# Performance work log

Hardware: AMD Instinct MI355X
Metric: run time of the kernel (lower is better)

Reference implementation:

```python
import jax, jax.numpy as jnp
import numpy as np

B = 64      # batch
T = 32      # frames per clip
H = 256     # hidden_dim
NMAX = 64   # max boxes per batch element


def _n_per_frame():
    rng = np.random.default_rng(0)
    return rng.integers(32, NMAX + 1, size=B)  # each n <= NMAX


def setup_inputs() -> dict:
    n = _n_per_frame()
    N = int(n.sum())  # total boxes across batch (~3072)
    key = jax.random.key(0)
    k1, k2, k3 = jax.random.split(key, 3)
    bbox = jax.random.uniform(k1, (N * T, 4), dtype=jnp.float32)
    W1 = jax.random.normal(k2, (4, 128), dtype=jnp.float32) * 0.5
    b1 = jnp.zeros((128,), jnp.float32)
    W2 = jax.random.normal(k3, (128, H), dtype=jnp.float32) * 0.0884  # ~1/sqrt(128)
    b2 = jnp.zeros((H,), jnp.float32)
    return {
        "bbox": bbox,
        "W1": W1, "b1": b1, "W2": W2, "b2": b2,
        "n_per_frame": jnp.asarray(n, jnp.int32),
        "n_max": NMAX,
    }


def reference(bbox, W1, b1, W2, b2, n_per_frame, n_max):
    N = bbox.shape[0] // T  # static total box count
    # tiny MLP: 4 -> 128 -> H
    pos = (jax.nn.relu(bbox @ W1 + b1) @ W2 + b2).reshape(N, T, H)
    # ragged scatter into padded (B*n_max, T, H) tensor
    frame_id = jnp.repeat(jnp.arange(B), n_per_frame, total_repeat_length=N)  # [N]
    starts = jnp.cumsum(n_per_frame) - n_per_frame                            # exclusive cumsum [B]
    local = jnp.arange(N) - starts[frame_id]                                  # slot within frame
    tgt = frame_id * n_max + local                                            # [N] unique targets
    pos_pad = jnp.zeros((B * n_max, T, H), pos.dtype).at[tgt].set(pos)
    # (B, n_max, T, H) -> (B, T, n_max, H) -> (B*T, n_max, H) -> (n_max, B*T, H)
    out = (pos_pad.reshape(B, n_max, T, H)
           .transpose(0, 2, 1, 3)
           .reshape(B * T, n_max, H)
           .transpose(1, 0, 2))
    return out
```

## Files before the change

### kernel.cpp

```cpp
#include <hip/hip_runtime.h>

#define B_ 64
#define T_ 32
#define H_ 256
#define HID_ 128
#define NMAX_ 64
#define TILES 2048
#define GRID 512
#define BLOCK 256

typedef __attribute__((ext_vector_type(8))) short short8;
typedef __attribute__((ext_vector_type(4))) float f32x4;

__device__ __forceinline__ short f2bf(float f) {
    unsigned u = __builtin_bit_cast(unsigned, f);
    u = (u + 0x7fffu + ((u >> 16) & 1u)) >> 16;
    return (short)u;
}

__global__ __launch_bounds__(BLOCK, 2)
void pe_fused(const float* __restrict__ bbox,
              const float* __restrict__ W1,
              const float* __restrict__ b1,
              const float* __restrict__ W2,
              const float* __restrict__ b2,
              const int*   __restrict__ npf,
              float* __restrict__ out,
              int NT)
{
    __shared__ float W1s[512];
    __shared__ float b1s[128];
    __shared__ short Hs[64 * 136];

    const int tid  = threadIdx.x;
    const int wave = tid >> 6;
    const int lane = tid & 63;
    const int q    = lane >> 4;
    const int m16  = lane & 15;

    if (tid < 256) { W1s[tid] = W1[tid]; W1s[tid + 256] = W1[tid + 256]; }
    if (tid < 128) b1s[tid] = b1[tid];

    short8 Bf[4][4];
    float  b2v[4];
#pragma unroll
    for (int ct = 0; ct < 4; ++ct) {
        const int n = wave * 64 + ct * 16 + m16;
        b2v[ct] = b2[n];
#pragma unroll
        for (int kc = 0; kc < 4; ++kc) {
            const int k0 = kc * 32 + q * 8;
            short8 f;
#pragma unroll
            for (int jj = 0; jj < 8; ++jj)
                f[jj] = f2bf(W2[(k0 + jj) * H_ + n]);
            Bf[ct][kc] = f;
        }
    }
    __syncthreads();

    const int r4 = tid >> 2;
    const int c4 = tid & 3;

    for (int tt = blockIdx.x; tt < TILES; tt += GRID) {
        const int b  = tt >> 5;
        const int j  = tt & 31;
        const int nb = npf[b];
        const int l0 = 2 * j;

        const int ob0 = (l0 * (B_ * T_) + b * T_) * H_;
        const int ob1 = ob0 + (B_ * T_) * H_;

        if (l0 >= nb) {
            const int s = r4 >> 5, t = r4 & 31;
            float* dst = out + (s ? ob1 : ob0) + t * H_ + c4 * 64;
            const float4 z = make_float4(0.f, 0.f, 0.f, 0.f);
#pragma unroll
            for (int w = 0; w < 16; ++w)
                *(float4*)(dst + w * 4) = z;
            continue;
        }

        int sb = 0;
        for (int x = 0; x < b; ++x) sb += npf[x];

        {
            const int gr = (sb + l0) * T_ + r4;
            float4 bb = make_float4(0.f, 0.f, 0.f, 0.f);
            if (gr < NT) bb = *(const float4*)(bbox + gr * 4);
#pragma unroll
            for (int w = 0; w < 4; ++w) {
                short8 hv;
#pragma unroll
                for (int jj = 0; jj < 8; ++jj) {
                    const int h = c4 * 32 + w * 8 + jj;
                    float v = b1s[h];
                    v = fmaf(bb.x, W1s[h],       v);
                    v = fmaf(bb.y, W1s[128 + h], v);
                    v = fmaf(bb.z, W1s[256 + h], v);
                    v = fmaf(bb.w, W1s[384 + h], v);
                    v = fmaxf(v, 0.f);
                    hv[jj] = f2bf(v);
                }
                *(short8*)&Hs[r4 * 136 + c4 * 32 + w * 8] = hv;
            }
        }
        __syncthreads();

        f32x4 acc[4][4];
#pragma unroll
        for (int rt = 0; rt < 4; ++rt)
#pragma unroll
            for (int ct = 0; ct < 4; ++ct)
                acc[rt][ct] = (f32x4){0.f, 0.f, 0.f, 0.f};

#pragma unroll
        for (int kc = 0; kc < 4; ++kc) {
            short8 a[4];
#pragma unroll
            for (int rt = 0; rt < 4; ++rt)
                a[rt] = *(const short8*)&Hs[(rt * 16 + m16) * 136 + kc * 32 + q * 8];
#pragma unroll
            for (int rt = 0; rt < 4; ++rt)
#pragma unroll
                for (int ct = 0; ct < 4; ++ct)
                    acc[rt][ct] = __builtin_amdgcn_mfma_f32_16x16x32_bf16(
                        a[rt], Bf[ct][kc], acc[rt][ct], 0, 0, 0);
        }
        __syncthreads();

        const bool v1 = (l0 + 1) < nb;
#pragma unroll
        for (int rt = 0; rt < 4; ++rt) {
#pragma unroll
            for (int reg = 0; reg < 4; ++reg) {
                const int rl = rt * 16 + q * 4 + reg;
                const int s = rl >> 5, t = rl & 31;
                const int base = (s ? ob1 : ob0) + t * H_;
                const bool ok = (s == 0) | v1;
#pragma unroll
                for (int ct = 0; ct < 4; ++ct) {
                    const int h = wave * 64 + ct * 16 + m16;
                    out[base + h] = ok ? (acc[rt][ct][reg] + b2v[ct]) : 0.f;
                }
            }
        }
    }
}

extern "C" void kernel_launch(void* const* d_in, const int* in_sizes, int n_in,
                              void* d_out, int out_size, void* d_ws, size_t ws_size,
                              hipStream_t stream)
{
    const float* bbox = (const float*)d_in[0];
    const float* W1   = (const float*)d_in[1];
    const float* b1   = (const float*)d_in[2];
    const float* W2   = (const float*)d_in[3];
    const float* b2   = (const float*)d_in[4];
    const int*   npf  = (const int*)d_in[5];
    const int NT = in_sizes[0] / 4;

    pe_fused<<<GRID, BLOCK, 0, stream>>>(bbox, W1, b1, W2, b2, npf,
                                         (float*)d_out, NT);
}
```

Baseline: 158.9 us.

## Precompute frame offsets in LDS, double-buffer hidden tile, coalesce zero stores

Computes the per-frame box counts and their exclusive prefix sums once per block with a wave shuffle scan and keeps them in shared memory. This replaces the serial per-tile loop over npf that recomputed each frame's start offset. The hidden-activation tile is now double-buffered, which lets the second __syncthreads per tile be dropped. Zero-fill stores for padded tiles are remapped so each wave writes whole contiguous rows, and shared memory use grows to hold the second buffer.

```diff
diff --git a/kernel.cpp b/kernel.cpp
--- a/kernel.cpp
+++ b/kernel.cpp
@@ -3,7 +3,6 @@
 #define B_ 64
 #define T_ 32
 #define H_ 256
-#define HID_ 128
 #define NMAX_ 64
 #define TILES 2048
 #define GRID 512
@@ -30,7 +29,9 @@
 {
     __shared__ float W1s[512];
     __shared__ float b1s[128];
-    __shared__ short Hs[64 * 136];
+    __shared__ int   s_n[64];
+    __shared__ int   s_start[64];
+    __shared__ short Hs[2][64 * 136];
 
     const int tid  = threadIdx.x;
     const int wave = tid >> 6;
@@ -40,6 +41,18 @@
 
     if (tid < 256) { W1s[tid] = W1[tid]; W1s[tid + 256] = W1[tid + 256]; }
     if (tid < 128) b1s[tid] = b1[tid];
+
+    if (wave == 0) {
+        int v = npf[lane];
+        s_n[lane] = v;
+        int s = v;
+#pragma unroll
+        for (int d = 1; d < 64; d <<= 1) {
+            int u = __shfl_up(s, d, 64);
+            if (lane >= d) s += u;
+        }
+        s_start[lane] = s - v;
+    }
 
     short8 Bf[4][4];
     float  b2v[4];
@@ -62,32 +75,34 @@
     const int r4 = tid >> 2;
     const int c4 = tid & 3;
 
+    int pbuf = 0;
+
     for (int tt = blockIdx.x; tt < TILES; tt += GRID) {
         const int b  = tt >> 5;
-        const int j  = tt & 31;
-        const int nb = npf[b];
-        const int l0 = 2 * j;
+        const int l0 = (tt & 31) * 2;
+        const int nb = s_n[b];
 
         const int ob0 = (l0 * (B_ * T_) + b * T_) * H_;
         const int ob1 = ob0 + (B_ * T_) * H_;
 
         if (l0 >= nb) {
-            const int s = r4 >> 5, t = r4 & 31;
-            float* dst = out + (s ? ob1 : ob0) + t * H_ + c4 * 64;
             const float4 z = make_float4(0.f, 0.f, 0.f, 0.f);
 #pragma unroll
-            for (int w = 0; w < 16; ++w)
-                *(float4*)(dst + w * 4) = z;
+            for (int rr = 0; rr < 16; ++rr) {
+                const int r = rr * 4 + wave;
+                float* dst = out + (r < 32 ? ob0 + r * H_ : ob1 + (r - 32) * H_);
+                *(float4*)(dst + lane * 4) = z;
+            }
             continue;
         }
 
-        int sb = 0;
-        for (int x = 0; x < b; ++x) sb += npf[x];
+        const int sb = s_start[b];
 
         {
             const int gr = (sb + l0) * T_ + r4;
             float4 bb = make_float4(0.f, 0.f, 0.f, 0.f);
             if (gr < NT) bb = *(const float4*)(bbox + gr * 4);
+            short* hrow = &Hs[pbuf][r4 * 136 + c4 * 32];
 #pragma unroll
             for (int w = 0; w < 4; ++w) {
                 short8 hv;
@@ -102,7 +117,7 @@
                     v = fmaxf(v, 0.f);
                     hv[jj] = f2bf(v);
                 }
-                *(short8*)&Hs[r4 * 136 + c4 * 32 + w * 8] = hv;
+                *(short8*)(hrow + w * 8) = hv;
             }
         }
         __syncthreads();
@@ -119,7 +134,7 @@
             short8 a[4];
 #pragma unroll
             for (int rt = 0; rt < 4; ++rt)
-                a[rt] = *(const short8*)&Hs[(rt * 16 + m16) * 136 + kc * 32 + q * 8];
+                a[rt] = *(const short8*)&Hs[pbuf][(rt * 16 + m16) * 136 + kc * 32 + q * 8];
 #pragma unroll
             for (int rt = 0; rt < 4; ++rt)
 #pragma unroll
@@ -127,7 +142,7 @@
                     acc[rt][ct] = __builtin_amdgcn_mfma_f32_16x16x32_bf16(
                         a[rt], Bf[ct][kc], acc[rt][ct], 0, 0, 0);
         }
-        __syncthreads();
+        pbuf ^= 1;
 
         const bool v1 = (l0 + 1) < nb;
 #pragma unroll
@@ -135,14 +150,12 @@
 #pragma unroll
             for (int reg = 0; reg < 4; ++reg) {
                 const int rl = rt * 16 + q * 4 + reg;
-                const int s = rl >> 5, t = rl & 31;
-                const int base = (s ? ob1 : ob0) + t * H_;
-                const bool ok = (s == 0) | v1;
+                const bool ok = (rl < 32) | v1;
+                float* dst = out + (rl < 32 ? ob0 + rl * H_ : ob1 + (rl - 32) * H_)
+                                 + wave * 64 + m16;
 #pragma unroll
-                for (int ct = 0; ct < 4; ++ct) {
-                    const int h = wave * 64 + ct * 16 + m16;
-                    out[base + h] = ok ? (acc[rt][ct][reg] + b2v[ct]) : 0.f;
-                }
+                for (int ct = 0; ct < 4; ++ct)
+                    dst[ct * 16] = ok ? (acc[rt][ct][reg] + b2v[ct]) : 0.f;
             }
         }
     }
```

New measurement: 157.2 us. No clear change (-1.1%).
